# Optimization experiments

Hardware: AMD Instinct MI355X
Metric: run time of the kernel (lower is better)

The kernel has to match this reference:

```python
import jax, jax.numpy as jnp
import numpy as np

B, C, S = 32, 256, 64  # batch, channels, spatial_size (h == w == S)


def _xavier(key, shape):
    fan_in, fan_out = shape[0], shape[1]
    bound = float(np.sqrt(6.0 / (fan_in + fan_out)))
    return jax.random.uniform(key, shape, jnp.float32, -bound, bound)


def setup_inputs() -> dict:
    key = jax.random.key(0)
    ks = jax.random.split(key, 7)
    x = jax.random.normal(ks[0], (B, C, S, S), dtype=jnp.float32)
    ww0 = _xavier(ks[1], (S, 1))
    ww1 = _xavier(ks[2], (S, 1))
    ww2 = _xavier(ks[3], (S, 1))
    hw0 = _xavier(ks[4], (S, 1))
    hw1 = _xavier(ks[5], (S, 1))
    hw2 = _xavier(ks[6], (S, 1))
    z = jnp.zeros((1, S), dtype=jnp.float32)
    return {
        'x': x,
        'ww0': ww0, 'ww1': ww1, 'ww2': ww2,
        'wb0': z, 'wb1': z, 'wb2': z,
        'hw0': hw0, 'hw1': hw1, 'hw2': hw2,
        'hb0': z, 'hb1': z, 'hb2': z,
    }


def _branch(mean_vec, max_vec, w0, w1, w2, b0, b1, b2):
    # mean_vec, max_vec: (b, S); w*: (S, 1); b*: (1, S)
    s = jax.nn.softmax(mean_vec, axis=1)          # (b, S)
    y0 = mean_vec @ w0                            # (b, 1)
    y1 = max_vec @ w1                             # (b, 1)
    y0_t = jnp.tanh(y0 * s + b0)                  # (b, S)
    y1_t = jnp.tanh(y1 * s + b1)                  # (b, S)
    return (y1_t @ w2) * y0_t + b2                # (b, S)


def reference(x, ww0, ww1, ww2, wb0, wb1, wb2, hw0, hw1, hw2, hb0, hb1, hb2):
    # x: (b, c, h, w) with h == w == S
    sp_max = jnp.max(x, axis=1)                   # (b, h, w)
    sp_mean = jnp.mean(x, axis=1)                 # (b, h, w)
    width_max = jnp.max(sp_max, axis=1)           # (b, w)
    width_mean = jnp.mean(sp_mean, axis=1)        # (b, w)
    height_max = jnp.max(sp_max, axis=2)          # (b, h)
    height_mean = jnp.mean(sp_mean, axis=2)       # (b, h)
    y_w = _branch(width_mean, width_max, ww0, ww1, ww2, wb0, wb1, wb2)   # (b, w)
    y_h = _branch(height_mean, height_max, hw0, hw1, hw2, hb0, hb1, hb2)  # (b, h)
    spatial = jnp.tanh(y_h[:, :, None] * y_w[:, None, :])[:, None]       # (b,1,h,w)
    return x * (spatial + 1.0)
```

## Files before the change

### kernel.cpp

```cpp
#include <hip/hip_runtime.h>
#include <float.h>

#define BB 32
#define CC 256
#define SS 64
#define IMG (SS * SS)
#define NPIX (BB * IMG)
#define NTOT (BB * CC * IMG)

typedef float f32x4 __attribute__((ext_vector_type(4)));

__device__ __forceinline__ f32x4 f4max(f32x4 a, f32x4 b) {
    f32x4 r;
    r.x = fmaxf(a.x, b.x); r.y = fmaxf(a.y, b.y);
    r.z = fmaxf(a.z, b.z); r.w = fmaxf(a.w, b.w);
    return r;
}

__global__ __launch_bounds__(256) void reduce_c_kernel(const float* __restrict__ x,
                                                       float* __restrict__ sp_max,
                                                       float* __restrict__ sp_mean) {
    const int blk   = blockIdx.x;
    const int b     = blk >> 4;
    const int chunk = blk & 15;
    const int tid   = threadIdx.x;
    const int wave  = tid >> 6;
    const int lane  = tid & 63;
    const int pos   = (chunk << 8) + (lane << 2);

    const float* xp = x + ((size_t)(b * CC + wave * 64) << 12) + pos;

    f32x4 vmax = (f32x4)(-FLT_MAX);
    f32x4 vsum = (f32x4)(0.f);
#pragma unroll 16
    for (int c = 0; c < 64; ++c) {
        f32x4 v = *(const f32x4*)(xp + ((size_t)c << 12));
        vmax = f4max(vmax, v);
        vsum += v;
    }

    __shared__ f32x4 smax[4][64];
    __shared__ f32x4 ssum[4][64];
    smax[wave][lane] = vmax;
    ssum[wave][lane] = vsum;
    __syncthreads();

    if (wave == 0) {
        f32x4 m = smax[0][lane];
        f32x4 s = ssum[0][lane];
#pragma unroll
        for (int w = 1; w < 4; ++w) {
            m = f4max(m, smax[w][lane]);
            s += ssum[w][lane];
        }
        const float inv = 1.0f / (float)CC;
        f32x4 mn = s * inv;
        *(f32x4*)(sp_max + (size_t)b * IMG + pos) = m;
        *(f32x4*)(sp_mean + (size_t)b * IMG + pos) = mn;
    }
}

__device__ __forceinline__ float allreduce_sum(float v) {
#pragma unroll
    for (int o = 32; o > 0; o >>= 1) v += __shfl_xor(v, o);
    return v;
}
__device__ __forceinline__ float allreduce_max(float v) {
#pragma unroll
    for (int o = 32; o > 0; o >>= 1) v = fmaxf(v, __shfl_xor(v, o));
    return v;
}

__device__ __forceinline__ float branch_lane(float meanv, float maxv,
                                             float w0, float w1, float w2,
                                             float b0, float b1, float b2) {
    float m  = allreduce_max(meanv);
    float e  = expf(meanv - m);
    float s  = e / allreduce_sum(e);
    float y0 = allreduce_sum(meanv * w0);
    float y1 = allreduce_sum(maxv * w1);
    float y0t = tanhf(fmaf(y0, s, b0));
    float y1t = tanhf(fmaf(y1, s, b1));
    float yw2 = allreduce_sum(y1t * w2);
    return fmaf(yw2, y0t, b2);
}

__global__ __launch_bounds__(64) void branch_kernel(
        const float* __restrict__ sp_max, const float* __restrict__ sp_mean,
        const float* __restrict__ ww0, const float* __restrict__ ww1, const float* __restrict__ ww2,
        const float* __restrict__ wb0, const float* __restrict__ wb1, const float* __restrict__ wb2,
        const float* __restrict__ hw0, const float* __restrict__ hw1, const float* __restrict__ hw2,
        const float* __restrict__ hb0, const float* __restrict__ hb1, const float* __restrict__ hb2,
        float* __restrict__ spatial) {
    const int b = blockIdx.x;
    const int t = threadIdx.x;
    const float* smx = sp_max + (size_t)b * IMG;
    const float* smn = sp_mean + (size_t)b * IMG;

    float wmax = -FLT_MAX, wsum = 0.f;
    float hmax = -FLT_MAX, hsum = 0.f;
#pragma unroll 4
    for (int i = 0; i < 64; ++i) {
        wmax = fmaxf(wmax, smx[i * 64 + t]);
        wsum += smn[i * 64 + t];
        hmax = fmaxf(hmax, smx[t * 64 + i]);
        hsum += smn[t * 64 + i];
    }
    const float inv = 1.0f / (float)SS;
    float y_w = branch_lane(wsum * inv, wmax, ww0[t], ww1[t], ww2[t], wb0[t], wb1[t], wb2[t]);
    float y_h = branch_lane(hsum * inv, hmax, hw0[t], hw1[t], hw2[t], hb0[t], hb1[t], hb2[t]);

    __shared__ float sh_h[64];
    sh_h[t] = y_h;
    __syncthreads();

    float* sp = spatial + (size_t)b * IMG;
#pragma unroll 4
    for (int h = 0; h < 64; ++h) {
        sp[h * 64 + t] = tanhf(sh_h[h] * y_w);
    }
}

__global__ __launch_bounds__(256) void apply_kernel(const float* __restrict__ x,
                                                    const float* __restrict__ spatial,
                                                    float* __restrict__ out) {
    const int n4 = NTOT / 4;
    const int stride = gridDim.x * blockDim.x;
    for (int i = blockIdx.x * blockDim.x + threadIdx.x; i < n4; i += stride) {
        const size_t base = (size_t)i << 2;
        f32x4 xv = ((const f32x4*)x)[i];
        const size_t b   = base >> 20;
        const size_t pos = base & (IMG - 1);
        f32x4 sv = *(const f32x4*)(spatial + (b << 12) + pos);
        f32x4 ov = xv * (sv + 1.0f);
        __builtin_nontemporal_store(ov, ((f32x4*)out) + i);
    }
}

extern "C" void kernel_launch(void* const* d_in, const int* in_sizes, int n_in,
                              void* d_out, int out_size, void* d_ws, size_t ws_size,
                              hipStream_t stream) {
    const float* x   = (const float*)d_in[0];
    const float* ww0 = (const float*)d_in[1];
    const float* ww1 = (const float*)d_in[2];
    const float* ww2 = (const float*)d_in[3];
    const float* wb0 = (const float*)d_in[4];
    const float* wb1 = (const float*)d_in[5];
    const float* wb2 = (const float*)d_in[6];
    const float* hw0 = (const float*)d_in[7];
    const float* hw1 = (const float*)d_in[8];
    const float* hw2 = (const float*)d_in[9];
    const float* hb0 = (const float*)d_in[10];
    const float* hb1 = (const float*)d_in[11];
    const float* hb2 = (const float*)d_in[12];
    float* out = (float*)d_out;

    float* sp_max  = (float*)d_ws;
    float* sp_mean = sp_max + NPIX;
    float* spatial = sp_mean + NPIX;

    reduce_c_kernel<<<NPIX / 256, 256, 0, stream>>>(x, sp_max, sp_mean);
    branch_kernel<<<BB, 64, 0, stream>>>(sp_max, sp_mean,
                                         ww0, ww1, ww2, wb0, wb1, wb2,
                                         hw0, hw1, hw2, hb0, hb1, hb2, spatial);
    apply_kernel<<<4096, 256, 0, stream>>>(x, spatial, out);
}
```

Baseline: 78.57 us.

## Fuse channel reduction with branch via last-block atomic counter

Merges the channel-reduction and branch kernels into one. Each block reduces its rows to partial width and height statistics, and the last block per batch (found through an atomic counter) finishes the branch MLPs and writes the spatial map. This removes a kernel launch and the full sp_max/sp_mean round trip through memory, at the cost of an extra memset and threadfence synchronisation. The apply kernel also now handles two float4 vectors per thread iteration.

```diff
diff --git a/kernel.cpp b/kernel.cpp
--- a/kernel.cpp
+++ b/kernel.cpp
@@ -10,54 +10,24 @@
 
 typedef float f32x4 __attribute__((ext_vector_type(4)));
 
+#define WPM_OFF 0
+#define WPS_OFF 32768
+#define HMX_OFF 65536
+#define HSM_OFF 67584
+#define SPA_OFF 69632
+#define CNT_BYTE_OFF ((SPA_OFF + NPIX) * 4)
+
 __device__ __forceinline__ f32x4 f4max(f32x4 a, f32x4 b) {
     f32x4 r;
     r.x = fmaxf(a.x, b.x); r.y = fmaxf(a.y, b.y);
     r.z = fmaxf(a.z, b.z); r.w = fmaxf(a.w, b.w);
     return r;
 }
-
-__global__ __launch_bounds__(256) void reduce_c_kernel(const float* __restrict__ x,
-                                                       float* __restrict__ sp_max,
-                                                       float* __restrict__ sp_mean) {
-    const int blk   = blockIdx.x;
-    const int b     = blk >> 4;
-    const int chunk = blk & 15;
-    const int tid   = threadIdx.x;
-    const int wave  = tid >> 6;
-    const int lane  = tid & 63;
-    const int pos   = (chunk << 8) + (lane << 2);
-
-    const float* xp = x + ((size_t)(b * CC + wave * 64) << 12) + pos;
-
-    f32x4 vmax = (f32x4)(-FLT_MAX);
-    f32x4 vsum = (f32x4)(0.f);
-#pragma unroll 16
-    for (int c = 0; c < 64; ++c) {
-        f32x4 v = *(const f32x4*)(xp + ((size_t)c << 12));
-        vmax = f4max(vmax, v);
-        vsum += v;
-    }
-
-    __shared__ f32x4 smax[4][64];
-    __shared__ f32x4 ssum[4][64];
-    smax[wave][lane] = vmax;
-    ssum[wave][lane] = vsum;
-    __syncthreads();
-
-    if (wave == 0) {
-        f32x4 m = smax[0][lane];
-        f32x4 s = ssum[0][lane];
-#pragma unroll
-        for (int w = 1; w < 4; ++w) {
-            m = f4max(m, smax[w][lane]);
-            s += ssum[w][lane];
-        }
-        const float inv = 1.0f / (float)CC;
-        f32x4 mn = s * inv;
-        *(f32x4*)(sp_max + (size_t)b * IMG + pos) = m;
-        *(f32x4*)(sp_mean + (size_t)b * IMG + pos) = mn;
-    }
+__device__ __forceinline__ f32x4 shfl_xor4(f32x4 v, int m) {
+    f32x4 r;
+    r.x = __shfl_xor(v.x, m); r.y = __shfl_xor(v.y, m);
+    r.z = __shfl_xor(v.z, m); r.w = __shfl_xor(v.w, m);
+    return r;
 }
 
 __device__ __forceinline__ float allreduce_sum(float v) {
@@ -85,55 +55,119 @@
     return fmaf(yw2, y0t, b2);
 }
 
-__global__ __launch_bounds__(64) void branch_kernel(
-        const float* __restrict__ sp_max, const float* __restrict__ sp_mean,
+__global__ __launch_bounds__(256) void reduce_branch_kernel(
+        const float* __restrict__ x,
         const float* __restrict__ ww0, const float* __restrict__ ww1, const float* __restrict__ ww2,
         const float* __restrict__ wb0, const float* __restrict__ wb1, const float* __restrict__ wb2,
         const float* __restrict__ hw0, const float* __restrict__ hw1, const float* __restrict__ hw2,
         const float* __restrict__ hb0, const float* __restrict__ hb1, const float* __restrict__ hb2,
-        float* __restrict__ spatial) {
-    const int b = blockIdx.x;
-    const int t = threadIdx.x;
-    const float* smx = sp_max + (size_t)b * IMG;
-    const float* smn = sp_mean + (size_t)b * IMG;
-
-    float wmax = -FLT_MAX, wsum = 0.f;
-    float hmax = -FLT_MAX, hsum = 0.f;
+        float* __restrict__ ws, int* __restrict__ cnt) {
+    const int blk  = blockIdx.x;
+    const int b    = blk >> 4;
+    const int j    = blk & 15;
+    const int tid  = threadIdx.x;
+    const int wave = tid >> 6;
+    const int lane = tid & 63;
+    const int pos0 = j << 8;
+
+    const float* xp = x + ((size_t)(b * CC + wave * 64) << 12) + pos0 + (lane << 2);
+    f32x4 vmax = (f32x4)(-FLT_MAX);
+    f32x4 vsum = (f32x4)(0.f);
+#pragma unroll 16
+    for (int c = 0; c < 64; ++c) {
+        f32x4 v = *(const f32x4*)(xp + ((size_t)c << 12));
+        vmax = f4max(vmax, v);
+        vsum += v;
+    }
+
+    __shared__ f32x4 smax[4][64];
+    __shared__ f32x4 ssum[4][64];
+    __shared__ float sh_w[64], sh_h[64];
+    __shared__ int islast;
+    smax[wave][lane] = vmax;
+    ssum[wave][lane] = vsum;
+    __syncthreads();
+
+    if (wave == 0) {
+        f32x4 m = smax[0][lane];
+        f32x4 s = ssum[0][lane];
+#pragma unroll
+        for (int w = 1; w < 4; ++w) {
+            m = f4max(m, smax[w][lane]);
+            s += ssum[w][lane];
+        }
+        f32x4 mean = s * (1.0f / (float)CC);
+
+        float em = fmaxf(fmaxf(m.x, m.y), fmaxf(m.z, m.w));
+        float es = mean.x + mean.y + mean.z + mean.w;
+#pragma unroll
+        for (int o = 1; o < 16; o <<= 1) {
+            em = fmaxf(em, __shfl_xor(em, o));
+            es += __shfl_xor(es, o);
+        }
+        if ((lane & 15) == 0) {
+            const int row = 4 * j + (lane >> 4);
+            ws[HMX_OFF + b * 64 + row] = em;
+            ws[HSM_OFF + b * 64 + row] = es;
+        }
+        f32x4 cm = m, cs = mean;
+        cm = f4max(cm, shfl_xor4(cm, 16));
+        cm = f4max(cm, shfl_xor4(cm, 32));
+        cs += shfl_xor4(cs, 16);
+        cs += shfl_xor4(cs, 32);
+        if (lane < 16) {
+            *(f32x4*)(ws + WPM_OFF + (b * 16 + j) * 64 + lane * 4) = cm;
+            *(f32x4*)(ws + WPS_OFF + (b * 16 + j) * 64 + lane * 4) = cs;
+        }
+    }
+    __syncthreads();
+    __threadfence();
+    if (tid == 0) islast = (atomicAdd(&cnt[b], 1) == 15) ? 1 : 0;
+    __syncthreads();
+    if (!islast) return;
+
+    __threadfence();
+    if (wave == 0) {
+        float wm = -FLT_MAX, wsv = 0.f;
+#pragma unroll
+        for (int j2 = 0; j2 < 16; ++j2) {
+            wm = fmaxf(wm, ws[WPM_OFF + (b * 16 + j2) * 64 + lane]);
+            wsv += ws[WPS_OFF + (b * 16 + j2) * 64 + lane];
+        }
+        sh_w[lane] = branch_lane(wsv * (1.0f / (float)SS), wm,
+                                 ww0[lane], ww1[lane], ww2[lane],
+                                 wb0[lane], wb1[lane], wb2[lane]);
+    } else if (wave == 1) {
+        float hm = ws[HMX_OFF + b * 64 + lane];
+        float hs = ws[HSM_OFF + b * 64 + lane];
+        sh_h[lane] = branch_lane(hs * (1.0f / (float)SS), hm,
+                                 hw0[lane], hw1[lane], hw2[lane],
+                                 hb0[lane], hb1[lane], hb2[lane]);
+    }
+    __syncthreads();
+    float* sp = ws + SPA_OFF + (size_t)b * IMG;
 #pragma unroll 4
-    for (int i = 0; i < 64; ++i) {
-        wmax = fmaxf(wmax, smx[i * 64 + t]);
-        wsum += smn[i * 64 + t];
-        hmax = fmaxf(hmax, smx[t * 64 + i]);
-        hsum += smn[t * 64 + i];
-    }
-    const float inv = 1.0f / (float)SS;
-    float y_w = branch_lane(wsum * inv, wmax, ww0[t], ww1[t], ww2[t], wb0[t], wb1[t], wb2[t]);
-    float y_h = branch_lane(hsum * inv, hmax, hw0[t], hw1[t], hw2[t], hb0[t], hb1[t], hb2[t]);
-
-    __shared__ float sh_h[64];
-    sh_h[t] = y_h;
-    __syncthreads();
-
-    float* sp = spatial + (size_t)b * IMG;
-#pragma unroll 4
-    for (int h = 0; h < 64; ++h) {
-        sp[h * 64 + t] = tanhf(sh_h[h] * y_w);
+    for (int p = tid; p < IMG; p += 256) {
+        sp[p] = tanhf(sh_h[p >> 6] * sh_w[p & 63]);
     }
 }
 
 __global__ __launch_bounds__(256) void apply_kernel(const float* __restrict__ x,
                                                     const float* __restrict__ spatial,
                                                     float* __restrict__ out) {
-    const int n4 = NTOT / 4;
+    const int nPairs = NTOT / 8;
     const int stride = gridDim.x * blockDim.x;
-    for (int i = blockIdx.x * blockDim.x + threadIdx.x; i < n4; i += stride) {
-        const size_t base = (size_t)i << 2;
-        f32x4 xv = ((const f32x4*)x)[i];
-        const size_t b   = base >> 20;
-        const size_t pos = base & (IMG - 1);
-        f32x4 sv = *(const f32x4*)(spatial + (b << 12) + pos);
-        f32x4 ov = xv * (sv + 1.0f);
-        __builtin_nontemporal_store(ov, ((f32x4*)out) + i);
+    for (int i = blockIdx.x * blockDim.x + threadIdx.x; i < nPairs; i += stride) {
+        const size_t e = (size_t)i << 3;
+        f32x4 xa = ((const f32x4*)x)[2 * (size_t)i];
+        f32x4 xb = ((const f32x4*)x)[2 * (size_t)i + 1];
+        const size_t b   = e >> 20;
+        const size_t pos = e & (IMG - 1);
+        const float* spp = spatial + (b << 12) + pos;
+        f32x4 sa = *(const f32x4*)(spp);
+        f32x4 sb = *(const f32x4*)(spp + 4);
+        __builtin_nontemporal_store(xa * (sa + 1.0f), ((f32x4*)out) + 2 * (size_t)i);
+        __builtin_nontemporal_store(xb * (sb + 1.0f), ((f32x4*)out) + 2 * (size_t)i + 1);
     }
 }
 
@@ -155,13 +189,15 @@
     const float* hb2 = (const float*)d_in[12];
     float* out = (float*)d_out;
 
-    float* sp_max  = (float*)d_ws;
-    float* sp_mean = sp_max + NPIX;
-    float* spatial = sp_mean + NPIX;
-
-    reduce_c_kernel<<<NPIX / 256, 256, 0, stream>>>(x, sp_max, sp_mean);
-    branch_kernel<<<BB, 64, 0, stream>>>(sp_max, sp_mean,
-                                         ww0, ww1, ww2, wb0, wb1, wb2,
-                                         hw0, hw1, hw2, hb0, hb1, hb2, spatial);
+    float* ws  = (float*)d_ws;
+    int*   cnt = (int*)((char*)d_ws + CNT_BYTE_OFF);
+    float* spatial = ws + SPA_OFF;
+
+    hipMemsetAsync(cnt, 0, BB * sizeof(int), stream);
+
+    reduce_branch_kernel<<<512, 256, 0, stream>>>(x,
+            ww0, ww1, ww2, wb0, wb1, wb2,
+            hw0, hw1, hw2, hb0, hb1, hb2,
+            ws, cnt);
     apply_kernel<<<4096, 256, 0, stream>>>(x, spatial, out);
 }
```

New measurement: 127.0 us. +61.6%, slower.
